# Optimization experiments

Hardware: AMD Instinct MI355X
Metric: run time of the kernel (lower is better)

Reference implementation:

```python
import jax, jax.numpy as jnp
import numpy as np

H = 1024
L = 2

def setup_inputs() -> dict:
    key = jax.random.key(0)
    k1, k2, k3, k4, k5 = jax.random.split(key, 5)
    B, S = 32, 2048
    scale = 1.0 / np.sqrt(H)
    return {
        "query": jax.random.normal(k1, (B, 1, H * L), dtype=jnp.float32),
        "keys": jax.random.normal(k2, (B, S, H), dtype=jnp.float32),
        "Wa_w": jax.random.normal(k3, (H * L, H), dtype=jnp.float32) * scale,
        "Wa_b": jnp.zeros((H,), dtype=jnp.float32),
        "Ua_w": jax.random.normal(k4, (H, H), dtype=jnp.float32) * scale,
        "Ua_b": jnp.zeros((H,), dtype=jnp.float32),
        "Va_w": jax.random.normal(k5, (H, 1), dtype=jnp.float32) * scale,
        "Va_b": jnp.zeros((1,), dtype=jnp.float32),
    }

def reference(query, keys, Wa_w, Wa_b, Ua_w, Ua_b, Va_w, Va_b):
    # query: [B,1,H*L], keys: [B,S,H]
    q = jnp.einsum('bqd,dh->bqh', query, Wa_w) + Wa_b   # [B,1,H]
    k = jnp.einsum('bsd,dh->bsh', keys, Ua_w) + Ua_b    # [B,S,H]
    e = jnp.tanh(q + k)                                  # [B,S,H]
    scores = jnp.einsum('bsh,ho->bso', e, Va_w) + Va_b   # [B,S,1]
    scores = scores[:, :, 0][:, None, :]                 # [B,1,S]
    weights = jax.nn.softmax(scores, axis=-1)            # [B,1,S]
    context = jnp.einsum('bqs,bsh->bqh', weights, keys)  # [B,1,H]
    return (context, weights)
```

## Files before the change

### kernel.cpp

```cpp
#include <hip/hip_runtime.h>
#include <hip/hip_bf16.h>


typedef __attribute__((ext_vector_type(8))) short short8;
typedef __attribute__((ext_vector_type(4))) float floatx4;

typedef const __attribute__((address_space(1))) unsigned int gu32;
typedef __attribute__((address_space(3))) unsigned int lu32;

__device__ __forceinline__ unsigned short f2bf(float f) {
    union { float f; unsigned int u; } c; c.f = f;
    unsigned int u = c.u + 0x7fffu + ((c.u >> 16) & 1u);
    return (unsigned short)(u >> 16);
}

__device__ __forceinline__ unsigned int f2bf2(float lo, float hi) {
#if __has_builtin(__builtin_amdgcn_cvt_pk_bf16_f32)
    auto r = __builtin_amdgcn_cvt_pk_bf16_f32(lo, hi);
    unsigned int u; __builtin_memcpy(&u, &r, 4);
    return u;
#else
    return (unsigned int)f2bf(lo) | ((unsigned int)f2bf(hi) << 16);
#endif
}

__device__ __forceinline__ void gld16(const unsigned short* g, unsigned short* l) {
    __builtin_amdgcn_global_load_lds(
        (gu32*)(uintptr_t)g,
        (lu32*)(unsigned int)(uintptr_t)l,
        16, 0, 0);
}

__global__ __launch_bounds__(256) void qproj_k(
    const float* __restrict__ query, const float* __restrict__ Wa,
    const float* __restrict__ Wab, const float* __restrict__ Uab,
    float* __restrict__ qws)
{
    __shared__ float qs[2048];
    __shared__ float red[16*64];
    const int tid = threadIdx.x;
    const int b = blockIdx.x, hc = blockIdx.y;
    #pragma unroll
    for (int i = 0; i < 8; i++) qs[tid + 256*i] = query[b*2048 + tid + 256*i];
    __syncthreads();
    const int hq = tid & 15;
    const int dg = tid >> 4;
    const float4* wp = reinterpret_cast<const float4*>(Wa + (size_t)(dg*128)*1024 + hc*64 + hq*4);
    const float* qp = qs + dg*128;
    float4 a0; a0.x = a0.y = a0.z = a0.w = 0.f;
    float4 a1; a1.x = a1.y = a1.z = a1.w = 0.f;
    #pragma unroll 4
    for (int d = 0; d < 128; d += 2) {
        float q0 = qp[d], q1 = qp[d+1];
        float4 w0 = wp[(size_t)d*256];
        float4 w1 = wp[(size_t)(d+1)*256];
        a0.x += q0*w0.x; a0.y += q0*w0.y; a0.z += q0*w0.z; a0.w += q0*w0.w;
        a1.x += q1*w1.x; a1.y += q1*w1.y; a1.z += q1*w1.z; a1.w += q1*w1.w;
    }
    a0.x += a1.x; a0.y += a1.y; a0.z += a1.z; a0.w += a1.w;
    *reinterpret_cast<float4*>(red + dg*64 + hq*4) = a0;
    __syncthreads();
    if (tid < 64) {
        float v = 0.f;
        #pragma unroll
        for (int g = 0; g < 16; g++) v += red[g*64 + tid];
        int hh = hc*64 + tid;
        qws[b*1024 + hh] = v + Wab[hh] + Uab[hh];
    }
}

__global__ __launch_bounds__(256) void uat_k(const float* __restrict__ Ua,
                                             unsigned short* __restrict__ uat)
{
    __shared__ unsigned short t[64][65];
    const int x = threadIdx.x & 63, yy = threadIdx.x >> 6;
    const int d0 = blockIdx.x*64, h0 = blockIdx.y*64;
    #pragma unroll
    for (int i = 0; i < 16; i++) {
        int y = yy*16 + i;
        t[y][x] = f2bf(Ua[(size_t)(d0+y)*1024 + h0 + x]);
    }
    __syncthreads();
    #pragma unroll
    for (int i = 0; i < 16; i++) {
        int y = yy*16 + i;
        uat[(size_t)(h0+y)*1024 + d0 + x] = t[x][y];
    }
}

__global__ __launch_bounds__(256) void score_gemm_fast(
    const float* __restrict__ keys,
    const unsigned short* __restrict__ uat,
    const float* __restrict__ qws,
    const float* __restrict__ Va,
    float* __restrict__ partial)
{
    __shared__ unsigned short aS[128*32];
    __shared__ unsigned short bS[128*32];
    const int tid = threadIdx.x;
    const int b = blockIdx.z;
    const int s0 = blockIdx.x * 128;
    const int h0 = blockIdx.y * 128;
    const int lane = tid & 63, wave = tid >> 6;
    const int quad = lane >> 4, l15 = lane & 15;
    const int wm = (wave & 1) * 64, wn = (wave >> 1) * 64;

    const int srow = lane >> 2;
    const int schunk = (lane & 3) ^ ((srow >> 1) & 3);

    floatx4 acc[4][4];
    #pragma unroll
    for (int i = 0; i < 4; i++)
        #pragma unroll
        for (int j = 0; j < 4; j++) acc[i][j] = (floatx4)0.0f;

    const float* kA = keys + (size_t)(b*2048 + s0)*1024;
    const unsigned short* ubase = uat + (size_t)h0*1024;
    const int c0 = wave*2, c1 = wave*2 + 1;
    const size_t boff0 = (size_t)(c0*16 + srow)*1024 + schunk*8;
    const size_t boff1 = (size_t)(c1*16 + srow)*1024 + schunk*8;

    const int arow0 = tid >> 2, ac = tid & 3;

    for (int k0 = 0; k0 < 1024; k0 += 32) {
        gld16(ubase + boff0 + k0, bS + c0*512);
        gld16(ubase + boff1 + k0, bS + c1*512);
        #pragma unroll
        for (int i = 0; i < 2; i++) {
            int row = arow0 + 64*i;
            int sl  = ac ^ ((row >> 1) & 3);
            const float* gp = kA + (size_t)row*1024 + k0 + ac*8;
            float4 v0 = *reinterpret_cast<const float4*>(gp);
            float4 v1 = *reinterpret_cast<const float4*>(gp + 4);
            uint4 w;
            w.x = f2bf2(v0.x, v0.y); w.y = f2bf2(v0.z, v0.w);
            w.z = f2bf2(v1.x, v1.y); w.w = f2bf2(v1.z, v1.w);
            *reinterpret_cast<uint4*>(aS + row*32 + sl*8) = w;
        }
        __syncthreads();
        short8 af[4], bf8[4];
        #pragma unroll
        for (int i = 0; i < 4; i++) {
            int row = wm + 16*i + l15;
            af[i] = *reinterpret_cast<const short8*>(aS + row*32 + ((quad ^ ((row>>1)&3)) * 8));
        }
        #pragma unroll
        for (int j = 0; j < 4; j++) {
            int row = wn + 16*j + l15;
            bf8[j] = *reinterpret_cast<const short8*>(bS + row*32 + ((quad ^ ((row>>1)&3)) * 8));
        }
        #pragma unroll
        for (int i = 0; i < 4; i++)
            #pragma unroll
            for (int j = 0; j < 4; j++)
                acc[i][j] = __builtin_amdgcn_mfma_f32_16x16x32_bf16(af[i], bf8[j], acc[i][j], 0, 0, 0);
        __syncthreads();
    }

    float qv[4], vav[4];
    #pragma unroll
    for (int j = 0; j < 4; j++) {
        int n = h0 + wn + 16*j + l15;
        qv[j]  = qws[b*1024 + n];
        vav[j] = Va[n];
    }
    const int slot = blockIdx.y * 2 + (wave >> 1);
    #pragma unroll
    for (int i = 0; i < 4; i++) {
        #pragma unroll
        for (int r = 0; r < 4; r++) {
            float p = 0.f;
            #pragma unroll
            for (int j = 0; j < 4; j++) {
                float x = qv[j] + acc[i][j][r];
                float e = __expf(2.f * x);
                float t = 1.f - 2.f * __builtin_amdgcn_rcpf(e + 1.f);
                p += vav[j] * t;
            }
            #pragma unroll
            for (int off = 1; off < 16; off <<= 1) p += __shfl_xor(p, off, 64);
            if (l15 == 0) {
                int m = wm + 16*i + quad*4 + r;
                partial[((size_t)b*16 + slot)*2048 + s0 + m] = p;
            }
        }
    }
}

__global__ __launch_bounds__(256) void softmax_k(const float* __restrict__ partial,
                                                 float* __restrict__ out_w)
{
    const int tid = threadIdx.x;
    const int b = blockIdx.x;
    __shared__ float wred[4], wred2[4];
    float sc[8];
    float mx = -3.0e38f;
    #pragma unroll
    for (int i = 0; i < 8; i++) {
        int s = tid + 256*i;
        float v = 0.f;
        #pragma unroll
        for (int ht = 0; ht < 16; ht++) v += partial[((size_t)b*16 + ht)*2048 + s];
        sc[i] = v; mx = fmaxf(mx, v);
    }
    #pragma unroll
    for (int off = 32; off >= 1; off >>= 1) mx = fmaxf(mx, __shfl_xor(mx, off, 64));
    if ((tid & 63) == 0) wred[tid >> 6] = mx;
    __syncthreads();
    mx = fmaxf(fmaxf(wred[0], wred[1]), fmaxf(wred[2], wred[3]));
    float e[8]; float lsum = 0.f;
    #pragma unroll
    for (int i = 0; i < 8; i++) { e[i] = __expf(sc[i] - mx); lsum += e[i]; }
    #pragma unroll
    for (int off = 32; off >= 1; off >>= 1) lsum += __shfl_xor(lsum, off, 64);
    if ((tid & 63) == 0) wred2[tid >> 6] = lsum;
    __syncthreads();
    float inv = 1.0f / (wred2[0] + wred2[1] + wred2[2] + wred2[3]);
    #pragma unroll
    for (int i = 0; i < 8; i++) out_w[b*2048 + tid + 256*i] = e[i] * inv;
}

__global__ __launch_bounds__(256) void ctx_k(const float* __restrict__ keys,
                                             const float* __restrict__ w,
                                             float* __restrict__ ctxp, int sper)
{
    const int tid = threadIdx.x;
    const int b = blockIdx.x, sc = blockIdx.y;
    const float4* k4 = reinterpret_cast<const float4*>(keys) + (size_t)(b*2048 + sc*sper)*256;
    const float* wp = w + b*2048 + sc*sper;
    float4 a; a.x = a.y = a.z = a.w = 0.f;
    #pragma unroll 4
    for (int s = 0; s < sper; s++) {
        float wv = wp[s];
        float4 kv = k4[(size_t)s*256 + tid];
        a.x += wv*kv.x; a.y += wv*kv.y; a.z += wv*kv.z; a.w += wv*kv.w;
    }
    reinterpret_cast<float4*>(ctxp)[((size_t)b*gridDim.y + sc)*256 + tid] = a;
}

__global__ __launch_bounds__(256) void ctxsum_k(const float* __restrict__ ctxp,
                                                float* __restrict__ out, int nc)
{
    const int idx = blockIdx.x*256 + threadIdx.x;
    const int b = idx >> 10, h = idx & 1023;
    float v = 0.f;
    for (int s = 0; s < nc; s++) v += ctxp[((size_t)b*nc + s)*1024 + h];
    out[idx] = v;
}

extern "C" void kernel_launch(void* const* d_in, const int* in_sizes, int n_in,
                              void* d_out, int out_size, void* d_ws, size_t ws_size,
                              hipStream_t stream)
{
    const float* query = (const float*)d_in[0];
    const float* keys  = (const float*)d_in[1];
    const float* Wa_w  = (const float*)d_in[2];
    const float* Wa_b  = (const float*)d_in[3];
    const float* Ua_w  = (const float*)d_in[4];
    const float* Ua_b  = (const float*)d_in[5];
    const float* Va_w  = (const float*)d_in[6];

    char* ws = (char*)d_ws;
    float*          qws     = (float*)(ws);
    unsigned short* uat     = (unsigned short*)(ws + (131072));
    float*          partial = (float*)(ws + (131072 + 2097152));
    float*          ctxp    = (float*)(ws + (131072 + 2097152 + 4194304));

    float* out_ctx = (float*)d_out;
    float* out_w   = out_ctx + 32*1024;

    qproj_k        <<<dim3(32, 16),    256, 0, stream>>>(query, Wa_w, Wa_b, Ua_b, qws);
    uat_k          <<<dim3(16, 16),    256, 0, stream>>>(Ua_w, uat);
    score_gemm_fast<<<dim3(16, 8, 32), 256, 0, stream>>>(keys, uat, qws, Va_w, partial);
    softmax_k      <<<dim3(32),        256, 0, stream>>>(partial, out_w);
    ctx_k          <<<dim3(32, 16),    256, 0, stream>>>(keys, out_w, ctxp, 128);
    ctxsum_k       <<<dim3(128),       256, 0, stream>>>(ctxp, out_ctx, 16);
}
```

Baseline: 655.1 us.

## Double-buffer score GEMM LDS tiles and prefetch next K-slice during MFMA

The score GEMM now keeps two LDS buffers for the keys and Ua^T tiles. The next K-slice is issued (direct global-to-LDS loads for B, register prefetch for A) before the MFMAs on the current slice run. The fp32-to-bf16 conversion and LDS store for the next A tile happen after the MFMAs, which cuts the loop to one barrier per iteration. Wave priority is also raised around the MFMA block. This doubles LDS use and raises register pressure, which could reduce occupancy.

```diff
diff --git a/kernel.cpp b/kernel.cpp
--- a/kernel.cpp
+++ b/kernel.cpp
@@ -95,8 +95,8 @@
     const float* __restrict__ Va,
     float* __restrict__ partial)
 {
-    __shared__ unsigned short aS[128*32];
-    __shared__ unsigned short bS[128*32];
+    __shared__ unsigned short aS[2][128*32];
+    __shared__ unsigned short bS[2][128*32];
     const int tid = threadIdx.x;
     const int b = blockIdx.z;
     const int s0 = blockIdx.x * 128;
@@ -122,39 +122,89 @@
 
     const int arow0 = tid >> 2, ac = tid & 3;
 
-    for (int k0 = 0; k0 < 1024; k0 += 32) {
-        gld16(ubase + boff0 + k0, bS + c0*512);
-        gld16(ubase + boff1 + k0, bS + c1*512);
+    gld16(ubase + boff0, bS[0] + c0*512);
+    gld16(ubase + boff1, bS[0] + c1*512);
+    #pragma unroll
+    for (int i = 0; i < 2; i++) {
+        int row = arow0 + 64*i;
+        int sl  = ac ^ ((row >> 1) & 3);
+        const float* gp = kA + (size_t)row*1024 + ac*8;
+        float4 v0 = *reinterpret_cast<const float4*>(gp);
+        float4 v1 = *reinterpret_cast<const float4*>(gp + 4);
+        uint4 w;
+        w.x = f2bf2(v0.x, v0.y); w.y = f2bf2(v0.z, v0.w);
+        w.z = f2bf2(v1.x, v1.y); w.w = f2bf2(v1.z, v1.w);
+        *reinterpret_cast<uint4*>(aS[0] + row*32 + sl*8) = w;
+    }
+    __syncthreads();
+
+    int cur = 0;
+    for (int kt = 0; kt < 31; ++kt) {
+        const int nxt = cur ^ 1;
+        const int k1 = (kt + 1) << 5;
+
+        gld16(ubase + boff0 + k1, bS[nxt] + c0*512);
+        gld16(ubase + boff1 + k1, bS[nxt] + c1*512);
+        float4 pa0[2], pa1[2];
         #pragma unroll
         for (int i = 0; i < 2; i++) {
             int row = arow0 + 64*i;
-            int sl  = ac ^ ((row >> 1) & 3);
-            const float* gp = kA + (size_t)row*1024 + k0 + ac*8;
-            float4 v0 = *reinterpret_cast<const float4*>(gp);
-            float4 v1 = *reinterpret_cast<const float4*>(gp + 4);
-            uint4 w;
-            w.x = f2bf2(v0.x, v0.y); w.y = f2bf2(v0.z, v0.w);
-            w.z = f2bf2(v1.x, v1.y); w.w = f2bf2(v1.z, v1.w);
-            *reinterpret_cast<uint4*>(aS + row*32 + sl*8) = w;
-        }
-        __syncthreads();
+            const float* gp = kA + (size_t)row*1024 + k1 + ac*8;
+            pa0[i] = *reinterpret_cast<const float4*>(gp);
+            pa1[i] = *reinterpret_cast<const float4*>(gp + 4);
+        }
+
         short8 af[4], bf8[4];
         #pragma unroll
         for (int i = 0; i < 4; i++) {
             int row = wm + 16*i + l15;
-            af[i] = *reinterpret_cast<const short8*>(aS + row*32 + ((quad ^ ((row>>1)&3)) * 8));
+            af[i] = *reinterpret_cast<const short8*>(aS[cur] + row*32 + ((quad ^ ((row>>1)&3)) * 8));
         }
         #pragma unroll
         for (int j = 0; j < 4; j++) {
             int row = wn + 16*j + l15;
-            bf8[j] = *reinterpret_cast<const short8*>(bS + row*32 + ((quad ^ ((row>>1)&3)) * 8));
-        }
+            bf8[j] = *reinterpret_cast<const short8*>(bS[cur] + row*32 + ((quad ^ ((row>>1)&3)) * 8));
+        }
+        __builtin_amdgcn_s_setprio(1);
         #pragma unroll
         for (int i = 0; i < 4; i++)
             #pragma unroll
             for (int j = 0; j < 4; j++)
                 acc[i][j] = __builtin_amdgcn_mfma_f32_16x16x32_bf16(af[i], bf8[j], acc[i][j], 0, 0, 0);
+        __builtin_amdgcn_s_setprio(0);
+
+        #pragma unroll
+        for (int i = 0; i < 2; i++) {
+            int row = arow0 + 64*i;
+            int sl  = ac ^ ((row >> 1) & 3);
+            uint4 w;
+            w.x = f2bf2(pa0[i].x, pa0[i].y); w.y = f2bf2(pa0[i].z, pa0[i].w);
+            w.z = f2bf2(pa1[i].x, pa1[i].y); w.w = f2bf2(pa1[i].z, pa1[i].w);
+            *reinterpret_cast<uint4*>(aS[nxt] + row*32 + sl*8) = w;
+        }
         __syncthreads();
+        cur = nxt;
+    }
+
+    {
+        short8 af[4], bf8[4];
+        #pragma unroll
+        for (int i = 0; i < 4; i++) {
+            int row = wm + 16*i + l15;
+            af[i] = *reinterpret_cast<const short8*>(aS[cur] + row*32 + ((quad ^ ((row>>1)&3)) * 8));
+        }
+        #pragma unroll
+        for (int j = 0; j < 4; j++) {
+            int row = wn + 16*j + l15;
+            bf8[j] = *reinterpret_cast<const short8*>(bS[cur] + row*32 + ((quad ^ ((row>>1)&3)) * 8));
+        }
+        __builtin_amdgcn_s_setprio(1);
+        #pragma unroll
+        for (int i = 0; i < 4; i++)
+            #pragma unroll
+            for (int j = 0; j < 4; j++)
+                acc[i][j] = __builtin_amdgcn_mfma_f32_16x16x32_bf16(af[i], bf8[j], acc[i][j], 0, 0, 0);
+        __builtin_amdgcn_s_setprio(0);
     }
 
     float qv[4], vav[4];
```

New measurement: 665.7 us. Within noise of the previous version (+1.6%).
